# Performance work log

Measured on AMD Instinct MI355X. Metric: run time of the kernel, lower is better.

The kernel has to match this reference:

```python
import jax, jax.numpy as jnp
import numpy as np

TOPK = 50
TEMP = 5.0

def _l2norm(x):
    return x / jnp.linalg.norm(x, axis=-1, keepdims=True)

def setup_inputs() -> dict:
    key = jax.random.key(0)
    k1, k2, k3 = jax.random.split(key, 3)
    b, m, d = 32, 196, 512
    n, c = 51, 1000
    return {
        "image_features": jax.random.normal(k1, (b, d), dtype=jnp.float32),
        "local_image_features": jax.random.normal(k2, (b, m, d), dtype=jnp.float32),
        "all_text_features": jax.random.normal(k3, (n, c, d), dtype=jnp.float32),
        "logit_scale": jnp.full((1,), 4.6052, dtype=jnp.float32),  # ln(100), CLIP default
    }

def reference(image_features, local_image_features, all_text_features, logit_scale):
    # Inference path of CustomCLIP.forward (labels=None) -> get_dense_logits2
    img = _l2norm(image_features)                 # [b, d]
    loc = _l2norm(local_image_features)           # [b, m, d]
    txt = _l2norm(all_text_features)              # [n, c, d]  (n = ndisc = 51)
    mean_txt = _l2norm(txt.mean(axis=0))          # [c, d]

    base_logits = img @ mean_txt.T                # [b, c]
    w_raw = jnp.einsum('bd,bmd->bm', img, loc)    # [b, m]
    txt_cnd = jnp.transpose(txt, (1, 0, 2))       # [c, n, d]
    v = jax.nn.softmax(jnp.einsum('cd,cnd->cn', mean_txt, txt_cnd) * TEMP, axis=1)  # [c, n]

    # similarity of every patch to every description, laid out with m last for top_k
    sim = jnp.einsum('bmd,cnd->bcnm', loc, txt_cnd)        # [b, c, n, m]
    sim_topk, idx_topk = jax.lax.top_k(sim, TOPK)          # [b, c, n, k] each

    b = img.shape[0]
    # gather per-image patch weights at selected patch indices: w_raw[b, idx]
    w_topk = w_raw[jnp.arange(b)[:, None, None, None], idx_topk]   # [b, c, n, k]
    w = jax.nn.softmax(w_topk * TEMP, axis=3)               # softmax over selected patches

    bias_logits = jnp.sum(sim_topk * w * v[None, :, :, None], axis=(2, 3))  # [b, c]
    return jnp.exp(logit_scale)[0] * (base_logits + bias_logits)
```

## Files before the change

### kernel.cpp

```cpp
#include <hip/hip_runtime.h>
#include <stdint.h>

typedef __bf16  bf16x8 __attribute__((ext_vector_type(8)));
typedef float   f32x4  __attribute__((ext_vector_type(4)));
typedef short   s16x2  __attribute__((ext_vector_type(2)));
typedef unsigned short u16;

#define TEMP 5.0f

__device__ inline float wsum(float v){
  #pragma unroll
  for (int off=32; off; off>>=1) v += __shfl_xor(v, off, 64);
  return v;
}
__device__ inline float wmax(float v){
  #pragma unroll
  for (int off=32; off; off>>=1) v = fmaxf(v, __shfl_xor(v, off, 64));
  return v;
}
__device__ inline u16 f2bf(float f){
  unsigned u = __float_as_uint(f);
  u = u + 0x7fffu + ((u>>16)&1u);
  return (u16)(u>>16);
}
__device__ inline float bfl(unsigned u){ return __uint_as_float(u<<16); }
__device__ inline float bfh(unsigned u){ return __uint_as_float(u & 0xffff0000u); }

__device__ inline s16x2 as_s16x2(int v){ union{int i; s16x2 v;} u; u.i=v; return u.v; }

__device__ inline s16x2 pkmin2(s16x2 a, s16x2 b){
  s16x2 r; r.x = a.x < b.x ? a.x : b.x; r.y = a.y < b.y ? a.y : b.y; return r;
}
__device__ inline s16x2 pkmax2(s16x2 a, s16x2 b){
  s16x2 r; r.x = a.x > b.x ? a.x : b.x; r.y = a.y > b.y ? a.y : b.y; return r;
}

#if __has_builtin(__builtin_amdgcn_mov_dpp)
__device__ inline int dxor1(int v){ return __builtin_amdgcn_mov_dpp(v, 0xB1, 0xF, 0xF, true); }
__device__ inline int dxor2(int v){ return __builtin_amdgcn_mov_dpp(v, 0x4E, 0xF, 0xF, true); }
#else
__device__ inline int dxor1(int v){ return __shfl_xor(v, 1, 64); }
__device__ inline int dxor2(int v){ return __shfl_xor(v, 2, 64); }
#endif

#if __has_builtin(__builtin_amdgcn_permlane16_swap)
__device__ inline int x16sum_i(int c){
  auto p = __builtin_amdgcn_permlane16_swap((unsigned)c, (unsigned)c, false, false);
  return (int)p[0] + (int)p[1];
}
__device__ inline int x16min_i(int c){
  auto p = __builtin_amdgcn_permlane16_swap((unsigned)c, (unsigned)c, false, false);
  return min((int)p[0], (int)p[1]);
}
__device__ inline int x16max_i(int c){
  auto p = __builtin_amdgcn_permlane16_swap((unsigned)c, (unsigned)c, false, false);
  return max((int)p[0], (int)p[1]);
}
__device__ inline float x16sum_f(float v){
  auto p = __builtin_amdgcn_permlane16_swap(__float_as_uint(v), __float_as_uint(v), false, false);
  return __uint_as_float(p[0]) + __uint_as_float(p[1]);
}
#else
__device__ inline int   x16sum_i(int c){ return c + __shfl_xor(c, 16, 64); }
__device__ inline int   x16min_i(int c){ return min(c, __shfl_xor(c, 16, 64)); }
__device__ inline int   x16max_i(int c){ return max(c, __shfl_xor(c, 16, 64)); }
__device__ inline float x16sum_f(float v){ return v + __shfl_xor(v, 16, 64); }
#endif

__device__ inline int ssum8_i(int c){ c += dxor1(c); c += dxor2(c); return x16sum_i(c); }
__device__ inline int smin8_i(int c){ c = min(c, dxor1(c)); c = min(c, dxor2(c)); return x16min_i(c); }
__device__ inline int smax8_i(int c){ c = max(c, dxor1(c)); c = max(c, dxor2(c)); return x16max_i(c); }
__device__ inline float ssum8_f(float v){
  v += __int_as_float(dxor1(__float_as_int(v)));
  v += __int_as_float(dxor2(__float_as_int(v)));
  return x16sum_f(v);
}

__device__ inline void cp16(void* lds_uniform, const void* g){
  __builtin_amdgcn_global_load_lds(
    (const __attribute__((address_space(1))) unsigned int*)g,
    (__attribute__((address_space(3))) unsigned int*)lds_uniform, 16, 0, 0);
}

__global__ void k_img(const float* __restrict__ X, float* __restrict__ imgn){
  int b = blockIdx.x, lane = threadIdx.x;
  const float* src = X + (size_t)b*512 + lane*8;
  float4 a = *(const float4*)src;
  float4 c = *(const float4*)(src+4);
  float ss = a.x*a.x+a.y*a.y+a.z*a.z+a.w*a.w + c.x*c.x+c.y*c.y+c.z*c.z+c.w*c.w;
  ss = wsum(ss);
  float inv = 1.0f/sqrtf(ss);
  float* dst = imgn + (size_t)b*512 + lane*8;
  float4 o0 = {a.x*inv,a.y*inv,a.z*inv,a.w*inv};
  float4 o1 = {c.x*inv,c.y*inv,c.z*inv,c.w*inv};
  *(float4*)dst = o0; *(float4*)(dst+4) = o1;
}

__global__ void k_txt(const float* __restrict__ X, u16* __restrict__ TXT, float* __restrict__ invn){
  int cn = blockIdx.x, lane = threadIdx.x;
  int kc = lane>>2, kk8 = (lane&3)*8;
  size_t dstE = ((size_t)kc*51008 + cn)*32 + kk8;
  if (cn >= 51000){
    uint4 z = {0,0,0,0};
    *(uint4*)(TXT + dstE) = z;
    return;
  }
  int c = cn/51, n = cn - c*51;
  const float* src = X + ((size_t)n*1000 + c)*512 + lane*8;
  float4 a = *(const float4*)src;
  float4 d = *(const float4*)(src+4);
  float ss = a.x*a.x+a.y*a.y+a.z*a.z+a.w*a.w + d.x*d.x+d.y*d.y+d.z*d.z+d.w*d.w;
  ss = wsum(ss);
  float inv = 1.0f/sqrtf(ss);
  u16 h0=f2bf(a.x*inv),h1=f2bf(a.y*inv),h2=f2bf(a.z*inv),h3=f2bf(a.w*inv);
  u16 h4=f2bf(d.x*inv),h5=f2bf(d.y*inv),h6=f2bf(d.z*inv),h7=f2bf(d.w*inv);
  uint4 o;
  o.x = (unsigned)h0 | ((unsigned)h1<<16);
  o.y = (unsigned)h2 | ((unsigned)h3<<16);
  o.z = (unsigned)h4 | ((unsigned)h5<<16);
  o.w = (unsigned)h6 | ((unsigned)h7<<16);
  *(uint4*)(TXT + dstE) = o;
  if (lane==0) invn[(size_t)n*1000 + c] = inv;
}

__global__ void k_mean(const float* __restrict__ X, const float* __restrict__ invn, float* __restrict__ MT){
  int c = blockIdx.x, tid = threadIdx.x, lane = tid&63, wv = tid>>6;
  __shared__ float sinv[51];
  __shared__ float red[4];
  if (tid < 51) sinv[tid] = invn[(size_t)tid*1000 + c];
  __syncthreads();
  int d0 = tid*2;
  float sx=0.f, sy=0.f;
  for (int n=0;n<51;++n){
    const float2 x = *(const float2*)(X + ((size_t)n*1000 + c)*512 + d0);
    float iv = sinv[n];
    sx += x.x*iv; sy += x.y*iv;
  }
  float ss = sx*sx + sy*sy;
  ss = wsum(ss);
  if (lane==0) red[wv] = ss;
  __syncthreads();
  float tot = red[0]+red[1]+red[2]+red[3];
  float inv = 1.0f/sqrtf(tot);
  float2 o = {sx*inv, sy*inv};
  *(float2*)(MT + (size_t)c*512 + d0) = o;
}

__global__ void k_v(const u16* __restrict__ TXT, const float* __restrict__ MT, float* __restrict__ vbuf){
  int c = blockIdx.x, lane = threadIdx.x;
  __shared__ float lg[51];
  const float* mp = MT + (size_t)c*512 + lane*8;
  float4 m0 = *(const float4*)mp;
  float4 m1 = *(const float4*)(mp+4);
  int kc = lane>>2, kk8 = (lane&3)*8;
  for (int n=0;n<51;++n){
    size_t e = ((size_t)kc*51008 + (size_t)(c*51+n))*32 + kk8;
    uint4 q = *(const uint4*)(TXT + e);
    float d = bfl(q.x)*m0.x + bfh(q.x)*m0.y + bfl(q.y)*m0.z + bfh(q.y)*m0.w
            + bfl(q.z)*m1.x + bfh(q.z)*m1.y + bfl(q.w)*m1.z + bfh(q.w)*m1.w;
    d = wsum(d);
    if (lane==0) lg[n] = d;
  }
  __syncthreads();
  float val = (lane<51) ? lg[lane] : -1e30f;
  float mx = wmax(val);
  float e = (lane<51) ? expf(TEMP*(val-mx)) : 0.f;
  float s = wsum(e);
  if (lane<51) vbuf[(size_t)c*51 + lane] = e/s;
}

__global__ void k_base(const float* __restrict__ imgn, const float* __restrict__ MT, float* __restrict__ bias){
  int c = blockIdx.x, lane = threadIdx.x;
  const float* mp = MT + (size_t)c*512 + lane*8;
  float4 m0 = *(const float4*)mp;
  float4 m1 = *(const float4*)(mp+4);
  for (int b=0;b<32;++b){
    const float* ip = imgn + (size_t)b*512 + lane*8;
    float4 i0 = *(const float4*)ip;
    float4 i1 = *(const float4*)(ip+4);
    float d = i0.x*m0.x+i0.y*m0.y+i0.z*m0.z+i0.w*m0.w
            + i1.x*m1.x+i1.y*m1.y+i1.z*m1.z+i1.w*m1.w;
    d = wsum(d);
    if (lane==0) bias[(size_t)b*1000 + c] = d;
  }
}

__global__ void k_loc(const float* __restrict__ L, const float* __restrict__ imgn,
                      u16* __restrict__ LOC, float* __restrict__ ewg){
  int m = blockIdx.x, b = blockIdx.y, lane = threadIdx.x;
  size_t dstE = ((size_t)(b*16 + (lane>>2))*224 + m)*32 + (lane&3)*8;
  if (m >= 196){
    uint4 z = {0,0,0,0};
    *(uint4*)(LOC + dstE) = z;
    if (lane==0) ewg[(size_t)b*224 + m] = 0.f;
    return;
  }
  const float* src = L + ((size_t)b*196 + m)*512 + lane*8;
  float4 a = *(const float4*)src;
  float4 d = *(const float4*)(src+4);
  const float* ip = imgn + (size_t)b*512 + lane*8;
  float4 i0 = *(const float4*)ip;
  float4 i1 = *(const float4*)(ip+4);
  float ss = a.x*a.x+a.y*a.y+a.z*a.z+a.w*a.w + d.x*d.x+d.y*d.y+d.z*d.z+d.w*d.w;
  float ws = a.x*i0.x+a.y*i0.y+a.z*i0.z+a.w*i0.w + d.x*i1.x+d.y*i1.y+d.z*i1.z+d.w*i1.w;
  ss = wsum(ss); ws = wsum(ws);
  float inv = 1.0f/sqrtf(ss);
  u16 h0=f2bf(a.x*inv),h1=f2bf(a.y*inv),h2=f2bf(a.z*inv),h3=f2bf(a.w*inv);
  u16 h4=f2bf(d.x*inv),h5=f2bf(d.y*inv),h6=f2bf(d.z*inv),h7=f2bf(d.w*inv);
  uint4 o;
  o.x = (unsigned)h0 | ((unsigned)h1<<16);
  o.y = (unsigned)h2 | ((unsigned)h3<<16);
  o.z = (unsigned)h4 | ((unsigned)h5<<16);
  o.w = (unsigned)h6 | ((unsigned)h7<<16);
  *(uint4*)(LOC + dstE) = o;
  if (lane==0) ewg[(size_t)b*224 + m] = expf(TEMP * ws * inv);
}

__global__ __launch_bounds__(512,8) void k_main(const u16* __restrict__ TXT, const u16* __restrict__ LOC,
                                                const float* __restrict__ ewg, const float* __restrict__ vbuf,
                                                float* __restrict__ bias){
  __shared__ __align__(16) char smem[30592];
  const int tid = threadIdx.x, lane = tid & 63, wv = tid >> 6;
  const int quad = lane >> 4, l16 = lane & 15;
  const int ns = wv >> 1, ms = wv & 1;
  const int lsw = lane ^ ((lane>>3)&3);
  const int qsw = (quad ^ ((l16>>1)&3)) * 16;
  const int sub = (lane & 3) | ((lane >> 2) & 4);
  const int col = ((lane >> 2) & 3) | ((lane >> 3) & 4);

  int id = blockIdx.x, b, cnt_;
  if (id < 24576){
    int g = id >> 10, r = id & 1023;
    b = r >> 5;  cnt_ = (g << 5) + (r & 31);
  } else {
    int r = id - 24576;
    b = r / 29;  cnt_ = 768 + r % 29;
  }
  const int cn0 = cnt_ * 64;

  float* ewl = (float*)(smem + 29696);
  if (tid < 224) ewl[tid] = ewg[(size_t)b*224 + tid];

  const f32x4 zero = {0.f,0.f,0.f,0.f};
  f32x4 acc[7];
  #pragma unroll
  for (int t=0;t<7;++t) acc[t]=zero;

  const u16* Abase = LOC + (size_t)(b*16)*224*32;
  char* Albd0 = smem;
  char* Albd1 = smem + 14336;

  auto stageA = [&](int kc, char* dst){
    const char* src = (const char*)(Abase + (size_t)kc*224*32);
    #pragma unroll
    for (int j=0;j<2;++j){
      int ch0 = j*512 + wv*64;
      if (ch0 < 896)
        cp16(dst + (size_t)ch0*16, src + (size_t)(ch0 + lsw)*16);
    }
  };
  auto loadB = [&](int kc)->bf16x8{
    size_t e = ((size_t)kc*51008 + (size_t)(cn0 + 16*ns + l16))*32 + quad*8;
    return *(const bf16x8*)(TXT + e);
  };
  auto domfma = [&](const char* Ab, bf16x8 bb){
    #pragma unroll
    for (int t=0;t<7;++t){
      bf16x8 af = *(const bf16x8*)(Ab + (size_t)((112*ms + 16*t + l16)*64) + qsw);
      acc[t] = __builtin_amdgcn_mfma_f32_16x16x32_bf16(af, bb, acc[t], 0,0,0);
    }
  };

  stageA(0, Albd0);
  bf16x8 bcur = loadB(0);
  __syncthreads();

  for (int kc = 0; kc < 16; ++kc){
    char* cur = (kc & 1) ? Albd1 : Albd0;
    char* nxt = (kc & 1) ? Albd0 : Albd1;
    bf16x8 bnext;
    if (kc < 15){
      stageA(kc+1, nxt);
      bnext = loadB(kc+1);
    }
    domfma(cur, bcur);
    bcur = bnext;
    __syncthreads();
  }

  const float KSC = 15360.0f;
  {
    unsigned* wr = (unsigned*)(void*)smem + (size_t)(ns*1856) + l16*116 + ms*56 + quad*2;
    #pragma unroll
    for (int t=0;t<7;++t){
      int a0 = (int)(acc[t][0]*KSC), a1 = (int)(acc[t][1]*KSC);
      int a2 = (int)(acc[t][2]*KSC), a3 = (int)(acc[t][3]*KSC);
      uint2 o; o.x = (unsigned)((a0 & 0xffff) | (a1<<16)); o.y = (unsigned)((a2 & 0xffff) | (a3<<16));
      *(uint2*)(wr + t*8) = o;
    }
  }
  __syncthreads();

  int kk[7][2];
  {
    const unsigned* rd = (const unsigned*)(void*)smem + (size_t)(ns*1856) + (8*ms + col)*116 + sub*14;
    #pragma unroll
    for (int j=0;j<7;++j){
      uint2 q = *(const uint2*)(rd + 2*j);
      kk[j][0] = (int)q.x;
      kk[j][1] = (int)q.y;
    }
  }
  const int PKPK = (int)0xC180C180;
  if (sub == 7){
    #pragma unroll
    for (int j=0;j<7;++j){ kk[j][0] = PKPK; kk[j][1] = PKPK; }
  }

  s16x2 vmn = as_s16x2(kk[0][0]), vmx = vmn;
  #pragma unroll
  for (int j=0;j<7;++j){
    #pragma unroll
    for (int i=0;i<2;++i){
      vmn = pkmin2(vmn, as_s16x2(kk[j][i]));
      vmx = pkmax2(vmx, as_s16x2(kk[j][i]));
    }
  }
  int kmn = min((int)vmn.x, (int)vmn.y);
  int kmx = max((int)vmx.x, (int)vmx.y);
  if (sub == 7){ kmn = 32000; kmx = -32000; }
  kmn = smin8_i(kmn);
  kmx = smax8_i(kmx);
  int lo = kmn - 1, hi = kmx + 1;

  float flo = 146.0f, fhi = -50.0f;
  int side = 0;
  bool done = false;

  #pragma unroll 1
  for (int it = 0; it < 14; ++it){
    float fr = flo * __builtin_amdgcn_rcpf(flo - fhi);
    fr = fminf(fmaxf(fr, 0.04f), 0.96f);
    int tm = lo + (int)(fr * (float)(hi - lo));
    tm = (tm <= lo) ? (lo + 1) : ((tm >= hi) ? (hi - 1) : tm);

    s16x2 tmv = as_s16x2((tm & 0xffff) | (tm << 16));
    s16x2 ca = {0,0};
    #pragma unroll
    for (int j=0;j<7;++j){
      ca = ca + ((as_s16x2(kk[j][0]) - tmv) >> 15);
      ca = ca + ((as_s16x2(kk[j][1]) - tmv) >> 15);
    }
    int clt = -((int)ca.x + (int)ca.y);
    int c = ssum8_i(28 - clt);

    bool ge = (c >= 50);
    if (!done){
      if (ge){ fhi = (side==1)  ? fhi*0.5f : fhi; flo = (float)(c-50); lo = tm; side = 1; }
      else   { flo = (side==-1) ? flo*0.5f : flo; fhi = (float)(c-50); hi = tm; side = -1; }
    }
    done = done || (c == 50) || ((hi - lo) <= 1);
    if (__all(done)) break;
  }
  const int thr = lo;

  float num = 0.f, den = 0.f;
  #pragma unroll
  for (int j=0;j<7;++j){
    float2 e0 = *(const float2*)(ewl + 28*sub + 4*j);
    float2 e1 = *(const float2*)(ewl + 28*sub + 4*j + 2);
    int a0 = (kk[j][0]<<16)>>16, a1 = kk[j][0]>>16;
    int a2 = (kk[j][1]<<16)>>16, a3 = kk[j][1]>>16;
    if (a0 >= thr){ num = fmaf((float)a0, e0.x, num); den += e0.x; }
    if (a1 >= thr){ num = fmaf((float)a1, e0.y, num); den += e0.y; }
    if (a2 >= thr){ num = fmaf((float)a2, e1.x, num); den += e1.x; }
    if (a3 >= thr){ num = fmaf((float)a3, e1.y, num); den += e1.y; }
  }
  num = ssum8_f(num);
  den = ssum8_f(den);

  int cn = cn0 + 16*ns + 8*ms + col;
  if (sub == 0 && cn < 51000){
    int c = cn/51;
    atomicAdd(bias + (size_t)b*1000 + c, vbuf[cn]*(num/(den*KSC)));
  }
}

__global__ void k_out(const float* __restrict__ bias, const float* __restrict__ ls, float* __restrict__ out){
  int i = blockIdx.x*256 + threadIdx.x;
  if (i < 32000){
    float sc = expf(ls[0]);
    out[i] = sc * bias[i];
  }
}

extern "C" void kernel_launch(void* const* d_in, const int* in_sizes, int n_in,
                              void* d_out, int out_size, void* d_ws, size_t ws_size,
                              hipStream_t stream) {
  const float* img = (const float*)d_in[0];
  const float* loc = (const float*)d_in[1];
  const float* txt = (const float*)d_in[2];
  const float* ls  = (const float*)d_in[3];
  char* ws = (char*)d_ws;
  float* imgn = (float*)(ws + 0);
  float* MT   = (float*)(ws + 65536);
  float* invn = (float*)(ws + 2113536);
  float* vbuf = (float*)(ws + 2317568);
  float* ewg  = (float*)(ws + 2521600);
  float* bias = (float*)(ws + 2550272);
  u16*   TXT  = (u16*)  (ws + 2678272);
  u16*   LOC  = (u16*)  (ws + 54910464);

  k_img <<<dim3(32),      dim3(64),  0, stream>>>(img, imgn);
  k_txt <<<dim3(51008),   dim3(64),  0, stream>>>(txt, TXT, invn);
  k_mean<<<dim3(1000),    dim3(256), 0, stream>>>(txt, invn, MT);
  k_v   <<<dim3(1000),    dim3(64),  0, stream>>>(TXT, MT, vbuf);
  k_base<<<dim3(1000),    dim3(64),  0, stream>>>(imgn, MT, bias);
  k_loc <<<dim3(224,32),  dim3(64),  0, stream>>>(loc, imgn, LOC, ewg);
  k_main<<<dim3(25504),   dim3(512), 0, stream>>>(TXT, LOC, ewg, vbuf, bias);
  k_out <<<dim3(125),     dim3(256), 0, stream>>>(bias, ls, (float*)d_out);
}
```

Measured before the change: 1.055 ms.

## Retile main GEMM warps to 4x2 M-by-N tiles and drop B prefetch

```diff
diff --git a/kernel.cpp b/kernel.cpp
--- a/kernel.cpp
+++ b/kernel.cpp
@@ -222,7 +222,8 @@
   __shared__ __align__(16) char smem[30592];
   const int tid = threadIdx.x, lane = tid & 63, wv = tid >> 6;
   const int quad = lane >> 4, l16 = lane & 15;
-  const int ns = wv >> 1, ms = wv & 1;
+  const int wm = wv >> 1, wn = wv & 1;
+  const int NT = (wm == 3) ? 2 : 4;
   const int lsw = lane ^ ((lane>>3)&3);
   const int qsw = (quad ^ ((l16>>1)&3)) * 16;
   const int sub = (lane & 3) | ((lane >> 2) & 4);
@@ -242,9 +243,9 @@
   if (tid < 224) ewl[tid] = ewg[(size_t)b*224 + tid];
 
   const f32x4 zero = {0.f,0.f,0.f,0.f};
-  f32x4 acc[7];
+  f32x4 acc[4][2];
   #pragma unroll
-  for (int t=0;t<7;++t) acc[t]=zero;
+  for (int t=0;t<4;++t){ acc[t][0]=zero; acc[t][1]=zero; }
 
   const u16* Abase = LOC + (size_t)(b*16)*224*32;
   char* Albd0 = smem;
@@ -259,51 +260,58 @@
         cp16(dst + (size_t)ch0*16, src + (size_t)(ch0 + lsw)*16);
     }
   };
-  auto loadB = [&](int kc)->bf16x8{
-    size_t e = ((size_t)kc*51008 + (size_t)(cn0 + 16*ns + l16))*32 + quad*8;
-    return *(const bf16x8*)(TXT + e);
+  struct B2 { bf16x8 x, y; };
+  auto loadB = [&](int kc)->B2{
+    B2 r;
+    size_t e = ((size_t)kc*51008 + (size_t)(cn0 + 32*wn + l16))*32 + quad*8;
+    r.x = *(const bf16x8*)(TXT + e);
+    r.y = *(const bf16x8*)(TXT + e + 16*32);
+    return r;
   };
-  auto domfma = [&](const char* Ab, bf16x8 bb){
-    #pragma unroll
-    for (int t=0;t<7;++t){
-      bf16x8 af = *(const bf16x8*)(Ab + (size_t)((112*ms + 16*t + l16)*64) + qsw);
-      acc[t] = __builtin_amdgcn_mfma_f32_16x16x32_bf16(af, bb, acc[t], 0,0,0);
+  auto domfma = [&](const char* Ab, B2 bb){
+    #pragma unroll
+    for (int t=0;t<4;++t){
+      if (t < NT){
+        bf16x8 af = *(const bf16x8*)(Ab + (size_t)(((4*wm + t)*16 + l16)*64) + qsw);
+        acc[t][0] = __builtin_amdgcn_mfma_f32_16x16x32_bf16(af, bb.x, acc[t][0], 0,0,0);
+        acc[t][1] = __builtin_amdgcn_mfma_f32_16x16x32_bf16(af, bb.y, acc[t][1], 0,0,0);
+      }
     }
   };
 
   stageA(0, Albd0);
-  bf16x8 bcur = loadB(0);
   __syncthreads();
 
   for (int kc = 0; kc < 16; ++kc){
     char* cur = (kc & 1) ? Albd1 : Albd0;
     char* nxt = (kc & 1) ? Albd0 : Albd1;
-    bf16x8 bnext;
-    if (kc < 15){
-      stageA(kc+1, nxt);
-      bnext = loadB(kc+1);
-    }
-    domfma(cur, bcur);
-    bcur = bnext;
+    B2 bb = loadB(kc);
+    if (kc < 15) stageA(kc+1, nxt);
+    domfma(cur, bb);
     __syncthreads();
   }
 
   const float KSC = 15360.0f;
   {
-    unsigned* wr = (unsigned*)(void*)smem + (size_t)(ns*1856) + l16*116 + ms*56 + quad*2;
-    #pragma unroll
-    for (int t=0;t<7;++t){
-      int a0 = (int)(acc[t][0]*KSC), a1 = (int)(acc[t][1]*KSC);
-      int a2 = (int)(acc[t][2]*KSC), a3 = (int)(acc[t][3]*KSC);
-      uint2 o; o.x = (unsigned)((a0 & 0xffff) | (a1<<16)); o.y = (unsigned)((a2 & 0xffff) | (a3<<16));
-      *(uint2*)(wr + t*8) = o;
+    #pragma unroll
+    for (int n=0;n<2;++n){
+      unsigned* wr = (unsigned*)(void*)smem + (size_t)((2*wn + n)*1856) + l16*116 + quad*2;
+      #pragma unroll
+      for (int t=0;t<4;++t){
+        if (t < NT){
+          int a0 = (int)(acc[t][n][0]*KSC), a1 = (int)(acc[t][n][1]*KSC);
+          int a2 = (int)(acc[t][n][2]*KSC), a3 = (int)(acc[t][n][3]*KSC);
+          uint2 o; o.x = (unsigned)((a0 & 0xffff) | (a1<<16)); o.y = (unsigned)((a2 & 0xffff) | (a3<<16));
+          *(uint2*)(wr + (4*wm + t)*8) = o;
+        }
+      }
     }
   }
   __syncthreads();
 
   int kk[7][2];
   {
-    const unsigned* rd = (const unsigned*)(void*)smem + (size_t)(ns*1856) + (8*ms + col)*116 + sub*14;
+    const unsigned* rd = (const unsigned*)(void*)smem + (size_t)((wv>>1)*1856) + ((wv&1)*8 + col)*116 + sub*14;
     #pragma unroll
     for (int j=0;j<7;++j){
       uint2 q = *(const uint2*)(rd + 2*j);
@@ -379,7 +387,7 @@
   num = ssum8_f(num);
   den = ssum8_f(den);
 
-  int cn = cn0 + 16*ns + 8*ms + col;
+  int cn = cn0 + (wv>>1)*16 + (wv&1)*8 + col;
   if (sub == 0 && cn < 51000){
     int c = cn/51;
     atomicAdd(bias + (size_t)b*1000 + c, vbuf[cn]*(num/(den*KSC)));
```

New measurement: 996.7 us. 5.6% less time.
